# Kernel optimization log

Hardware: AMD Instinct MI355X
Metric: run time of the kernel (lower is better)

The kernel has to match this reference:

```python
import jax, jax.numpy as jnp
import numpy as np

N, D_IN, D_OUT = 128, 512, 512
B = 256

def setup_inputs() -> dict:
    key = jax.random.key(0)
    kx, kw, kb = jax.random.split(key, 3)
    x = jax.random.normal(kx, (B, N, D_IN), dtype=jnp.float32)
    # nn.Linear default init: uniform(-1/sqrt(d_in), 1/sqrt(d_in)) for weight and bias
    bound = 1.0 / np.sqrt(D_IN)
    weight = jax.random.uniform(kw, (N, D_IN, D_OUT), dtype=jnp.float32, minval=-bound, maxval=bound)
    bias = jax.random.uniform(kb, (N, D_OUT), dtype=jnp.float32, minval=-bound, maxval=bound)
    return {"x": x, "weight": weight, "bias": bias}

def reference(x, weight, bias):
    # per-position linear: out[b,n,o] = sum_i x[b,n,i] * W[n,i,o] + bias[n,o]
    out = jnp.einsum('bni,nio->bno', x, weight)
    return out + bias[None]
```

## Files before the change

### kernel.cpp

```cpp
#include <hip/hip_runtime.h>

typedef __attribute__((ext_vector_type(8))) __bf16 bf16x8;
typedef __attribute__((ext_vector_type(4))) float f32x4;
typedef __attribute__((ext_vector_type(2))) float f32x2;

#define DI 512
#define DO 512
#define XROW (128 * DI)
#define OROW (128 * DO)
#define BK 32
#define BOFF 16384
#define BUFSZ 32768

#define VMCNT(n) asm volatile("s_waitcnt vmcnt(" #n ")" ::: "memory")
#define LGKM0()  asm volatile("s_waitcnt lgkmcnt(0)" ::: "memory")
#define SBAR()   __builtin_amdgcn_s_barrier()
#define SCHED0() __builtin_amdgcn_sched_barrier(0)

__global__ __launch_bounds__(512, 4)
void nlinear_mfma(const float* __restrict__ xp, const float* __restrict__ wp,
                  const float* __restrict__ bp, float* __restrict__ op) {
  int blk = blockIdx.x;
  int L = ((blk & 7) << 6) + (blk >> 3);
  int n = L >> 2, mt = (L >> 1) & 1, ot = L & 1;
  int mBase = mt << 7, oBase = ot << 8;

  __shared__ char lds[2 * BUFSZ];

  int tid = threadIdx.x, lane = tid & 63, wid = tid >> 6;
  int wm = (wid >> 2) << 6, wn = (wid & 3) << 6;
  int l16 = lane & 15, l4 = lane >> 4;

  unsigned aOff[2];
  #pragma unroll
  for (int i = 0; i < 2; ++i) {
    int r0 = (wid << 4) + (i << 3);
    int row = r0 + (lane >> 3);
    int g = (lane & 7) ^ ((row >> 1) & 7);
    aOff[i] = (unsigned)(((mBase + row) * XROW + n * DI) * 4 + g * 16);
  }
  auto gloadA = [&](int bufOff, int kt) {
    #pragma unroll
    for (int i = 0; i < 2; ++i) {
      int r0 = (wid << 4) + (i << 3);
      __builtin_amdgcn_global_load_lds(
          (const __attribute__((address_space(1))) void*)
              ((const char*)xp + aOff[i] + (unsigned)(kt * 128)),
          (__attribute__((address_space(3))) void*)(lds + bufOff + r0 * 128),
          16, 0, 0);
    }
  };

  int bo2 = (tid & 127) << 1, kq = tid >> 7;
  const float* bSrc = wp + ((size_t)n * DI + (kq << 3)) * DO + oBase + bo2;
  int bWr0 = BOFF + (bo2)     * 64 + ((kq ^ ((bo2 >> 1) & 3)) << 4);
  int bWr1 = BOFF + (bo2 + 1) * 64 + ((kq ^ ((bo2 >> 1) & 3)) << 4);

  f32x2 bRv[8];
  auto loadB = [&](int kt) {
    #pragma unroll
    for (int j = 0; j < 8; ++j)
      bRv[j] = *(const f32x2*)(bSrc + (size_t)(kt * BK + j) * DO);
  };
  auto writeB = [&](int bufOff) {
    bf16x8 v0, v1;
    #pragma unroll
    for (int j = 0; j < 8; ++j) { v0[j] = (__bf16)bRv[j].x; v1[j] = (__bf16)bRv[j].y; }
    *(bf16x8*)(lds + bufOff + bWr0) = v0;
    *(bf16x8*)(lds + bufOff + bWr1) = v1;
  };

  f32x4 acc[4][4];
  #pragma unroll
  for (int i = 0; i < 4; ++i)
    #pragma unroll
    for (int j = 0; j < 4; ++j)
      acc[i][j] = f32x4{0.f, 0.f, 0.f, 0.f};

  bf16x8 af[4];
  auto loadAfrags = [&](int bufOff) {
    #pragma unroll
    for (int i = 0; i < 4; ++i) {
      int row = wm + i * 16 + l16;
      int v7 = (row >> 1) & 7;
      const char* rb = lds + bufOff + row * 128;
      f32x4 lo = *(const f32x4*)(rb + ((((l4 << 1))     ^ v7) << 4));
      f32x4 hi = *(const f32x4*)(rb + ((((l4 << 1) | 1) ^ v7) << 4));
      af[i][0] = (__bf16)lo.x; af[i][1] = (__bf16)lo.y;
      af[i][2] = (__bf16)lo.z; af[i][3] = (__bf16)lo.w;
      af[i][4] = (__bf16)hi.x; af[i][5] = (__bf16)hi.y;
      af[i][6] = (__bf16)hi.z; af[i][7] = (__bf16)hi.w;
    }
  };
  auto computeJ = [&](int bufOff, int j) {
    int row = wn + j * 16 + l16;
    int slot = l4 ^ ((row >> 1) & 3);
    bf16x8 bfr = *(const bf16x8*)(lds + bufOff + BOFF + row * 64 + slot * 16);
    #pragma unroll
    for (int i = 0; i < 4; ++i)
      acc[i][j] = __builtin_amdgcn_mfma_f32_16x16x32_bf16(af[i], bfr, acc[i][j], 0, 0, 0);
  };

  float bi[4];
  #pragma unroll
  for (int j = 0; j < 4; ++j)
    bi[j] = bp[n * DO + oBase + wn + j * 16 + l16];

  gloadA(0, 0);
  loadB(0);
  writeB(0);
  loadB(1);
  SCHED0(); LGKM0(); SBAR(); SCHED0();

  for (int kt = 0; kt < 14; ++kt) {
    int curOff = (kt & 1) * BUFSZ, nxtOff = curOff ^ BUFSZ;
    loadAfrags(curOff);
    computeJ(curOff, 0);
    computeJ(curOff, 1);
    gloadA(nxtOff, kt + 1);
    writeB(nxtOff);
    loadB(kt + 2);
    SCHED0();
    computeJ(curOff, 2);
    computeJ(curOff, 3);
    SCHED0();
    VMCNT(8);
    LGKM0(); SBAR(); SCHED0();
  }
  {
    loadAfrags(0);
    computeJ(0, 0); computeJ(0, 1);
    gloadA(BUFSZ, 15);
    writeB(BUFSZ);
    SCHED0();
    computeJ(0, 2); computeJ(0, 3);
    SCHED0();
    VMCNT(0);
    LGKM0(); SBAR(); SCHED0();
  }
  loadAfrags(BUFSZ);
  computeJ(BUFSZ, 0); computeJ(BUFSZ, 1);
  computeJ(BUFSZ, 2); computeJ(BUFSZ, 3);

  #pragma unroll
  for (int i = 0; i < 4; ++i) {
    #pragma unroll
    for (int j = 0; j < 4; ++j) {
      #pragma unroll
      for (int r = 0; r < 4; ++r) {
        int m = mBase + wm + i * 16 + l4 * 4 + r;
        int o = oBase + wn + j * 16 + l16;
        op[(size_t)m * OROW + n * DO + o] = acc[i][j][r] + bi[j];
      }
    }
  }
}

extern "C" void kernel_launch(void* const* d_in, const int* in_sizes, int n_in,
                              void* d_out, int out_size, void* d_ws, size_t ws_size,
                              hipStream_t stream) {
  const float* x = (const float*)d_in[0];
  const float* w = (const float*)d_in[1];
  const float* b = (const float*)d_in[2];
  float* o = (float*)d_out;
  hipLaunchKernelGGL(nlinear_mfma, dim3(512), dim3(512), 0, stream, x, w, b, o);
}
```

Measured before the change: 45.51 us.

## Triple-buffer A tiles in LDS and split B into a separate double buffer

Reorganizes LDS into three 16KB A buffers plus a separate double-buffered B region, 80KB of dynamic shared memory in total. A tiles are now prefetched two k-steps ahead with direct global-to-LDS loads. B is loaded into registers one step ahead and converted to bf16 after all MFMAs of the current step. The aim is to hide more of the x-load latency and to batch all four MFMA groups together. The trade-offs are a shorter prefetch distance for B, which may expose weight-load latency when writeB waits on registers, and a larger LDS footprint that could limit occupancy.

```diff
diff --git a/kernel.cpp b/kernel.cpp
--- a/kernel.cpp
+++ b/kernel.cpp
@@ -9,8 +9,9 @@
 #define XROW (128 * DI)
 #define OROW (128 * DO)
 #define BK 32
-#define BOFF 16384
-#define BUFSZ 32768
+#define ABUF 16384
+#define BBASE 49152
+#define BBUF 16384
 
 #define VMCNT(n) asm volatile("s_waitcnt vmcnt(" #n ")" ::: "memory")
 #define LGKM0()  asm volatile("s_waitcnt lgkmcnt(0)" ::: "memory")
@@ -25,7 +26,7 @@
   int n = L >> 2, mt = (L >> 1) & 1, ot = L & 1;
   int mBase = mt << 7, oBase = ot << 8;
 
-  __shared__ char lds[2 * BUFSZ];
+  extern __shared__ char lds[];
 
   int tid = threadIdx.x, lane = tid & 63, wid = tid >> 6;
   int wm = (wid >> 2) << 6, wn = (wid & 3) << 6;
@@ -53,8 +54,8 @@
 
   int bo2 = (tid & 127) << 1, kq = tid >> 7;
   const float* bSrc = wp + ((size_t)n * DI + (kq << 3)) * DO + oBase + bo2;
-  int bWr0 = BOFF + (bo2)     * 64 + ((kq ^ ((bo2 >> 1) & 3)) << 4);
-  int bWr1 = BOFF + (bo2 + 1) * 64 + ((kq ^ ((bo2 >> 1) & 3)) << 4);
+  int bWr0 = (bo2)     * 64 + ((kq ^ ((bo2 >> 1) & 3)) << 4);
+  int bWr1 = (bo2 + 1) * 64 + ((kq ^ ((bo2 >> 1) & 3)) << 4);
 
   f32x2 bRv[8];
   auto loadB = [&](int kt) {
@@ -95,7 +96,7 @@
   auto computeJ = [&](int bufOff, int j) {
     int row = wn + j * 16 + l16;
     int slot = l4 ^ ((row >> 1) & 3);
-    bf16x8 bfr = *(const bf16x8*)(lds + bufOff + BOFF + row * 64 + slot * 16);
+    bf16x8 bfr = *(const bf16x8*)(lds + bufOff + row * 64 + slot * 16);
     #pragma unroll
     for (int i = 0; i < 4; ++i)
       acc[i][j] = __builtin_amdgcn_mfma_f32_16x16x32_bf16(af[i], bfr, acc[i][j], 0, 0, 0);
@@ -106,41 +107,46 @@
   for (int j = 0; j < 4; ++j)
     bi[j] = bp[n * DO + oBase + wn + j * 16 + l16];
 
+  loadB(0);
   gloadA(0, 0);
-  loadB(0);
-  writeB(0);
-  loadB(1);
-  SCHED0(); LGKM0(); SBAR(); SCHED0();
+  gloadA(ABUF, 1);
+  writeB(BBASE);
+  SCHED0();
+  VMCNT(2);
+  LGKM0(); SBAR(); SCHED0();
 
+  int aC = 0, aN = ABUF, aG = 2 * ABUF;
   for (int kt = 0; kt < 14; ++kt) {
-    int curOff = (kt & 1) * BUFSZ, nxtOff = curOff ^ BUFSZ;
-    loadAfrags(curOff);
-    computeJ(curOff, 0);
-    computeJ(curOff, 1);
-    gloadA(nxtOff, kt + 1);
-    writeB(nxtOff);
-    loadB(kt + 2);
+    int bC = BBASE + (kt & 1) * BBUF;
+    int bN = BBASE + ((kt + 1) & 1) * BBUF;
+    loadB(kt + 1);
+    gloadA(aG, kt + 2);
     SCHED0();
-    computeJ(curOff, 2);
-    computeJ(curOff, 3);
+    loadAfrags(aC);
+    computeJ(bC, 0); computeJ(bC, 1); computeJ(bC, 2); computeJ(bC, 3);
+    writeB(bN);
     SCHED0();
-    VMCNT(8);
+    VMCNT(2);
     LGKM0(); SBAR(); SCHED0();
+    int t = aC; aC = aN; aN = aG; aG = t;
   }
   {
-    loadAfrags(0);
-    computeJ(0, 0); computeJ(0, 1);
-    gloadA(BUFSZ, 15);
-    writeB(BUFSZ);
+    int bC = BBASE + (14 & 1) * BBUF, bN = BBASE + (15 & 1) * BBUF;
+    loadB(15);
     SCHED0();
-    computeJ(0, 2); computeJ(0, 3);
+    loadAfrags(aC);
+    computeJ(bC, 0); computeJ(bC, 1); computeJ(bC, 2); computeJ(bC, 3);
+    writeB(bN);
     SCHED0();
     VMCNT(0);
     LGKM0(); SBAR(); SCHED0();
+    int t = aC; aC = aN; aN = aG; aG = t;
   }
-  loadAfrags(BUFSZ);
-  computeJ(BUFSZ, 0); computeJ(BUFSZ, 1);
-  computeJ(BUFSZ, 2); computeJ(BUFSZ, 3);
+  {
+    int bC = BBASE + (15 & 1) * BBUF;
+    loadAfrags(aC);
+    computeJ(bC, 0); computeJ(bC, 1); computeJ(bC, 2); computeJ(bC, 3);
+  }
 
   #pragma unroll
   for (int i = 0; i < 4; ++i) {
@@ -163,5 +169,6 @@
   const float* w = (const float*)d_in[1];
   const float* b = (const float*)d_in[2];
   float* o = (float*)d_out;
-  hipLaunchKernelGGL(nlinear_mfma, dim3(512), dim3(512), 0, stream, x, w, b, o);
+  hipLaunchKernelGGL(nlinear_mfma, dim3(512), dim3(512), 81920, stream,
+                     x, w, b, o);
 }
```

Result: slower. 60.61 us (+33.2%).

## Load A fragments directly from global memory instead of staging through LDS

Applied to the files above, without the earlier changes.

Removes the LDS staging path for the activation tile (global_load_lds plus LDS reads) and has each lane load its A fragment straight from global memory into registers, converting to bf16 there. The LDS footprint is halved to hold only double-buffered weight tiles, and the explicit vmcnt waits are dropped in favour of compiler-managed waits. This trades LDS traffic and memory for redundant global reads, since the four wave columns each re-read the same A rows, and the global load latency is now exposed right before the MFMAs with no software prefetch.

```diff
diff --git a/kernel.cpp b/kernel.cpp
--- a/kernel.cpp
+++ b/kernel.cpp
@@ -9,10 +9,8 @@
 #define XROW (128 * DI)
 #define OROW (128 * DO)
 #define BK 32
-#define BOFF 16384
-#define BUFSZ 32768
+#define BBUF 16384
 
-#define VMCNT(n) asm volatile("s_waitcnt vmcnt(" #n ")" ::: "memory")
 #define LGKM0()  asm volatile("s_waitcnt lgkmcnt(0)" ::: "memory")
 #define SBAR()   __builtin_amdgcn_s_barrier()
 #define SCHED0() __builtin_amdgcn_sched_barrier(0)
@@ -25,36 +23,18 @@
   int n = L >> 2, mt = (L >> 1) & 1, ot = L & 1;
   int mBase = mt << 7, oBase = ot << 8;
 
-  __shared__ char lds[2 * BUFSZ];
+  __shared__ char lds[2 * BBUF];
 
   int tid = threadIdx.x, lane = tid & 63, wid = tid >> 6;
   int wm = (wid >> 2) << 6, wn = (wid & 3) << 6;
   int l16 = lane & 15, l4 = lane >> 4;
 
-  unsigned aOff[2];
-  #pragma unroll
-  for (int i = 0; i < 2; ++i) {
-    int r0 = (wid << 4) + (i << 3);
-    int row = r0 + (lane >> 3);
-    int g = (lane & 7) ^ ((row >> 1) & 7);
-    aOff[i] = (unsigned)(((mBase + row) * XROW + n * DI) * 4 + g * 16);
-  }
-  auto gloadA = [&](int bufOff, int kt) {
-    #pragma unroll
-    for (int i = 0; i < 2; ++i) {
-      int r0 = (wid << 4) + (i << 3);
-      __builtin_amdgcn_global_load_lds(
-          (const __attribute__((address_space(1))) void*)
-              ((const char*)xp + aOff[i] + (unsigned)(kt * 128)),
-          (__attribute__((address_space(3))) void*)(lds + bufOff + r0 * 128),
-          16, 0, 0);
-    }
-  };
+  const float* aB = xp + (size_t)(mBase + wm + l16) * XROW + n * DI + l4 * 8;
 
   int bo2 = (tid & 127) << 1, kq = tid >> 7;
   const float* bSrc = wp + ((size_t)n * DI + (kq << 3)) * DO + oBase + bo2;
-  int bWr0 = BOFF + (bo2)     * 64 + ((kq ^ ((bo2 >> 1) & 3)) << 4);
-  int bWr1 = BOFF + (bo2 + 1) * 64 + ((kq ^ ((bo2 >> 1) & 3)) << 4);
+  int bWr0 = (bo2)     * 64 + ((kq ^ ((bo2 >> 1) & 3)) << 4);
+  int bWr1 = (bo2 + 1) * 64 + ((kq ^ ((bo2 >> 1) & 3)) << 4);
 
   f32x2 bRv[8];
   auto loadB = [&](int kt) {
@@ -78,24 +58,10 @@
       acc[i][j] = f32x4{0.f, 0.f, 0.f, 0.f};
 
   bf16x8 af[4];
-  auto loadAfrags = [&](int bufOff) {
-    #pragma unroll
-    for (int i = 0; i < 4; ++i) {
-      int row = wm + i * 16 + l16;
-      int v7 = (row >> 1) & 7;
-      const char* rb = lds + bufOff + row * 128;
-      f32x4 lo = *(const f32x4*)(rb + ((((l4 << 1))     ^ v7) << 4));
-      f32x4 hi = *(const f32x4*)(rb + ((((l4 << 1) | 1) ^ v7) << 4));
-      af[i][0] = (__bf16)lo.x; af[i][1] = (__bf16)lo.y;
-      af[i][2] = (__bf16)lo.z; af[i][3] = (__bf16)lo.w;
-      af[i][4] = (__bf16)hi.x; af[i][5] = (__bf16)hi.y;
-      af[i][6] = (__bf16)hi.z; af[i][7] = (__bf16)hi.w;
-    }
-  };
   auto computeJ = [&](int bufOff, int j) {
     int row = wn + j * 16 + l16;
     int slot = l4 ^ ((row >> 1) & 3);
-    bf16x8 bfr = *(const bf16x8*)(lds + bufOff + BOFF + row * 64 + slot * 16);
+    bf16x8 bfr = *(const bf16x8*)(lds + bufOff + row * 64 + slot * 16);
     #pragma unroll
     for (int i = 0; i < 4; ++i)
       acc[i][j] = __builtin_amdgcn_mfma_f32_16x16x32_bf16(af[i], bfr, acc[i][j], 0, 0, 0);
@@ -106,41 +72,39 @@
   for (int j = 0; j < 4; ++j)
     bi[j] = bp[n * DO + oBase + wn + j * 16 + l16];
 
-  gloadA(0, 0);
   loadB(0);
   writeB(0);
   loadB(1);
   SCHED0(); LGKM0(); SBAR(); SCHED0();
 
-  for (int kt = 0; kt < 14; ++kt) {
-    int curOff = (kt & 1) * BUFSZ, nxtOff = curOff ^ BUFSZ;
-    loadAfrags(curOff);
+  for (int kt = 0; kt < 16; ++kt) {
+    int curOff = (kt & 1) * BBUF;
+    int nxtOff = curOff ^ BBUF;
+
+    #pragma unroll
+    for (int i = 0; i < 4; ++i) {
+      const float* ap = aB + i * (16 * XROW) + kt * BK;
+      f32x4 lo = *(const f32x4*)(ap);
+      f32x4 hi = *(const f32x4*)(ap + 4);
+      af[i][0] = (__bf16)lo.x; af[i][1] = (__bf16)lo.y;
+      af[i][2] = (__bf16)lo.z; af[i][3] = (__bf16)lo.w;
+      af[i][4] = (__bf16)hi.x; af[i][5] = (__bf16)hi.y;
+      af[i][6] = (__bf16)hi.z; af[i][7] = (__bf16)hi.w;
+    }
+
     computeJ(curOff, 0);
     computeJ(curOff, 1);
-    gloadA(nxtOff, kt + 1);
-    writeB(nxtOff);
-    loadB(kt + 2);
-    SCHED0();
+    if (kt < 15) {
+      writeB(nxtOff);
+      if (kt < 14) loadB(kt + 2);
+      SCHED0();
+    }
     computeJ(curOff, 2);
     computeJ(curOff, 3);
-    SCHED0();
-    VMCNT(8);
-    LGKM0(); SBAR(); SCHED0();
+    if (kt < 15) {
+      SCHED0(); LGKM0(); SBAR(); SCHED0();
+    }
   }
-  {
-    loadAfrags(0);
-    computeJ(0, 0); computeJ(0, 1);
-    gloadA(BUFSZ, 15);
-    writeB(BUFSZ);
-    SCHED0();
-    computeJ(0, 2); computeJ(0, 3);
-    SCHED0();
-    VMCNT(0);
-    LGKM0(); SBAR(); SCHED0();
-  }
-  loadAfrags(BUFSZ);
-  computeJ(BUFSZ, 0); computeJ(BUFSZ, 1);
-  computeJ(BUFSZ, 2); computeJ(BUFSZ, 3);
 
   #pragma unroll
   for (int i = 0; i < 4; ++i) {
```

Result: slower. 89.85 us (+97.4%).
